# Kernel optimization log

Hardware: AMD Instinct MI355X
Metric: run time of the kernel (lower is better)

## Reference

```python
import jax, jax.numpy as jnp
import numpy as np

B, T, D = 2, 1024, 1024
H, HKV = 16, 8
HD = D // H           # 64
NREP = H // HKV       # 2
NLAYERS = 3
MAXKV = T * NLAYERS   # 3072
EPS = 1e-5


def setup_inputs() -> dict:
    key = jax.random.key(0)
    ks = jax.random.split(key, 8)
    # rotary tables over full accumulated-KV range
    inv_freq = 1.0 / (10000.0 ** (jnp.arange(0, HD, 2, dtype=jnp.float32) / HD))  # (HD/2,)
    t = jnp.arange(MAXKV, dtype=jnp.float32)
    freqs = jnp.outer(t, inv_freq)  # (MAXKV, HD/2)
    return {
        "x": jax.random.normal(ks[0], (B, T, D), jnp.float32),
        "cos": jnp.cos(freqs),
        "sin": jnp.sin(freqs),
        "q_w": jax.random.normal(ks[1], (NLAYERS, D, D), jnp.float32) * 0.02,
        "k_w": jax.random.normal(ks[2], (NLAYERS, D // NREP, D), jnp.float32) * 0.02,
        "v_w": jax.random.normal(ks[3], (NLAYERS, D // NREP, D), jnp.float32) * 0.02,
        "ln_w": jnp.ones((NLAYERS, D), jnp.float32),
        "lam": jax.random.normal(ks[4], (NLAYERS,), jnp.float32) * 0.1,
        "out_w": jax.random.normal(ks[5], (D, D), jnp.float32) * 0.02,
        "final_ln_w": jnp.ones((D,), jnp.float32),
        "alpha": jnp.ones((1,), jnp.float32),
    }


def rmsnorm(x, w):
    return x * jax.lax.rsqrt(jnp.mean(x * x, axis=-1, keepdims=True) + EPS) * w


def rope(x, cos, sin):
    # x: (B, L, h, HD); cos/sin: (MAXKV, HD/2); flash_attn non-interleaved rotary
    L = x.shape[1]
    c = jnp.concatenate([cos[:L], cos[:L]], axis=-1)[None, :, None, :]
    s = jnp.concatenate([sin[:L], sin[:L]], axis=-1)[None, :, None, :]
    x1, x2 = jnp.split(x, 2, axis=-1)
    rot = jnp.concatenate([-x2, x1], axis=-1)
    return x * c + rot * s


def reference(x, cos, sin, q_w, k_w, v_w, ln_w, lam, out_w, final_ln_w, alpha):
    scale = HD ** -0.5
    # lambda weights: layernorm over sigmoid of the 3 scalars (biased var, eps=1e-5)
    s = jax.nn.sigmoid(lam)
    lw = (s - s.mean()) * jax.lax.rsqrt(s.var() + EPS)
    qidx = jnp.arange(T)
    k_list, v_list = [], []
    acc = jnp.zeros_like(x)
    for i in range(NLAYERS):
        q = (x @ q_w[i].T).reshape(B, T, H, HD)
        k = (x @ k_w[i].T).reshape(B, T, HKV, HD)
        v = (x @ v_w[i].T).reshape(B, T, HKV, HD)
        k_list.append(k)
        v_list.append(v)
        K = jnp.concatenate(k_list, axis=1)  # (B, L, HKV, HD), L=(i+1)*T
        V = jnp.concatenate(v_list, axis=1)
        L = K.shape[1]
        qr = rope(q, cos, sin)
        Kr = rope(K, cos, sin)  # whole buffer re-rotated each layer, as in original
        Kr = jnp.repeat(Kr, NREP, axis=2)  # GQA expand
        Vr = jnp.repeat(V, NREP, axis=2)
        scores = jnp.einsum('bqhd,bkhd->bhqk', qr, Kr) * scale
        # flash_attn causal=True with kv_len > q_len aligns bottom-right
        mask = jnp.arange(L)[None, :] <= (qidx + (L - T))[:, None]
        scores = jnp.where(mask[None, None], scores, -jnp.inf)
        attn = jax.nn.softmax(scores, axis=-1)
        o = jnp.einsum('bhqk,bkhd->bqhd', attn, Vr).reshape(B, T, D)
        acc = acc + rmsnorm(o, ln_w[i]) * lw[i]
    out = rmsnorm(acc + alpha * x, final_ln_w)
    return out @ out_w.T
```

## Files before the change

kernel.cpp:

```cpp
#include <hip/hip_runtime.h>
#include <type_traits>
#include <utility>

typedef unsigned short u16;
typedef unsigned int u32;
typedef short short8 __attribute__((ext_vector_type(8)));
typedef short s16x4 __attribute__((ext_vector_type(4)));
typedef __bf16 bf16x8 __attribute__((ext_vector_type(8)));
typedef float floatx4 __attribute__((ext_vector_type(4)));

template <typename V, typename = void> struct MfmaTakes : std::false_type {};
template <typename V>
struct MfmaTakes<V, std::void_t<decltype(__builtin_amdgcn_mfma_f32_16x16x32_bf16(
    std::declval<V>(), std::declval<V>(), std::declval<floatx4>(), 0, 0, 0))>>
    : std::true_type {};

template <typename V>
__device__ __forceinline__ floatx4 mfma_impl(V a, V b, floatx4 c, std::true_type) {
  return __builtin_amdgcn_mfma_f32_16x16x32_bf16(a, b, c, 0, 0, 0);
}
template <typename V>
__device__ __forceinline__ floatx4 mfma_impl(V a, V b, floatx4 c, std::false_type) {
  return __builtin_amdgcn_mfma_f32_16x16x32_bf16(
      __builtin_bit_cast(bf16x8, a), __builtin_bit_cast(bf16x8, b), c, 0, 0, 0);
}
__device__ __forceinline__ floatx4 MFMA16(short8 a, short8 b, floatx4 c) {
  return mfma_impl<short8>(a, b, c, MfmaTakes<short8>{});
}

__device__ __forceinline__ floatx4 MFMAK16(s16x4 a, s16x4 b, floatx4 c) {
  return __builtin_amdgcn_mfma_f32_16x16x16bf16_1k(a, b, c, 0, 0, 0);
}

#if defined(__has_builtin)
#if __has_builtin(__builtin_amdgcn_exp2f)
#define EXP2(x) __builtin_amdgcn_exp2f(x)
#else
#define EXP2(x) exp2f(x)
#endif
#else
#define EXP2(x) exp2f(x)
#endif

__device__ __forceinline__ u16 f2bf(float f) {
  union { float f; unsigned u; } x; x.f = f;
  unsigned r = (x.u + 0x7fffu + ((x.u >> 16) & 1u)) >> 16;
  return (u16)r;
}
__device__ __forceinline__ float bf2f(u16 v) {
  union { unsigned u; float f; } x; x.u = ((unsigned)v) << 16; return x.f;
}
__device__ __forceinline__ u32 packbf(float lo, float hi) {
  return (__float_as_uint(hi) & 0xffff0000u) | (__float_as_uint(lo) >> 16);
}
__device__ __forceinline__ u32 pack2bf(float lo, float hi) {
  return ((u32)f2bf(hi) << 16) | (u32)f2bf(lo);
}

#if defined(__has_builtin)
#if __has_builtin(__builtin_amdgcn_global_load_lds)
#define HAS_GLLDS 1
#endif
#endif
__device__ __forceinline__ void stage16(const u16* g, u16* lbase, int lane) {
#ifdef HAS_GLLDS
  __builtin_amdgcn_global_load_lds(
      (__attribute__((address_space(1))) void*)(g),
      (__attribute__((address_space(3))) void*)(lbase), 16, 0, 0);
#else
  *(uint4*)(lbase + lane * 8) = *(const uint4*)g;
#endif
}

#define QSCALE 0.18033688011112042f

__global__ __launch_bounds__(256) void prep_kernel(
    const float* __restrict__ x, const float* __restrict__ qw,
    const float* __restrict__ kw, const float* __restrict__ vw,
    const float* __restrict__ outw, const float* __restrict__ lam,
    u16* __restrict__ xb, u16* __restrict__ wcat, u16* __restrict__ outwb,
    float* __restrict__ lwbuf) {
  size_t gid = (size_t)blockIdx.x * 256 + threadIdx.x;
  if (gid == 0) {
    float s0 = 1.f / (1.f + expf(-lam[0]));
    float s1 = 1.f / (1.f + expf(-lam[1]));
    float s2 = 1.f / (1.f + expf(-lam[2]));
    float mean = (s0 + s1 + s2) * (1.f / 3.f);
    float d0 = s0 - mean, d1 = s1 - mean, d2 = s2 - mean;
    float var = (d0 * d0 + d1 * d1 + d2 * d2) * (1.f / 3.f);
    float r = rsqrtf(var + 1e-5f);
    lwbuf[0] = d0 * r; lwbuf[1] = d1 * r; lwbuf[2] = d2 * r;
  }
  if (gid < 524288) {
    float4 v = ((const float4*)x)[gid];
    ushort4 o; o.x = f2bf(v.x); o.y = f2bf(v.y); o.z = f2bf(v.z); o.w = f2bf(v.w);
    ((ushort4*)xb)[gid] = o;
    return;
  }
  size_t g2 = gid - 524288;
  if (g2 < 1572864) {
    int col4 = (int)(g2 & 255);
    int n = (int)(g2 >> 8);
    int layer = n >> 11, r = n & 2047;
    const float* srcrow;
    if (r < 1024) srcrow = qw + ((size_t)(layer * 1024 + r) << 10);
    else if (r < 1536) srcrow = kw + ((size_t)(layer * 512 + (r - 1024)) << 10);
    else srcrow = vw + ((size_t)(layer * 512 + (r - 1536)) << 10);
    float4 v = ((const float4*)srcrow)[col4];
    ushort4 o; o.x = f2bf(v.x); o.y = f2bf(v.y); o.z = f2bf(v.z); o.w = f2bf(v.w);
    ((ushort4*)wcat)[g2] = o;
    return;
  }
  size_t g3 = g2 - 1572864;
  if (g3 < 262144) {
    float4 v = ((const float4*)outw)[g3];
    ushort4 o; o.x = f2bf(v.x); o.y = f2bf(v.y); o.z = f2bf(v.z); o.w = f2bf(v.w);
    ((ushort4*)outwb)[g3] = o;
  }
}

__global__ __launch_bounds__(256) void gemm_qkv(
    const u16* __restrict__ A, const u16* __restrict__ Bw,
    const float* __restrict__ cosb, const float* __restrict__ sinb,
    u16* __restrict__ qr, u16* __restrict__ kr, u16* __restrict__ vt) {
  __shared__ u16 As[128][64];
  __shared__ u16 Bs[128][64];
  const unsigned flat = blockIdx.x;
  const int bm = (flat >> 3) & 15;
  const int bn = ((flat >> 7) << 3) + (flat & 7);
  const int tid = threadIdx.x;
  const int wave = tid >> 6, lane = tid & 63;
  const int quad = lane >> 4, l16 = lane & 15;
  const int wm = wave & 1, wn = wave >> 1;
  const int srow = lane >> 3, skc = (lane & 7) * 8;
  floatx4 acc[4][4];
#pragma unroll
  for (int i = 0; i < 4; i++)
#pragma unroll
    for (int j = 0; j < 4; j++) { acc[i][j][0] = 0.f; acc[i][j][1] = 0.f; acc[i][j][2] = 0.f; acc[i][j][3] = 0.f; }
  const u16* Abase = A + (size_t)(bm * 128) * 1024;
  const u16* Bbase = Bw + (size_t)(bn * 128) * 1024;
  for (int k0 = 0; k0 < 1024; k0 += 64) {
    __syncthreads();
#pragma unroll
    for (int i = 0; i < 4; i++) {
      int ch = wave * 4 + i;
      stage16(Abase + (size_t)(ch * 8 + srow) * 1024 + k0 + skc, &As[ch * 8][0], lane);
      stage16(Bbase + (size_t)(ch * 8 + srow) * 1024 + k0 + skc, &Bs[ch * 8][0], lane);
    }
    __syncthreads();
#pragma unroll
    for (int kf = 0; kf < 2; kf++) {
      short8 af[4], bf[4];
#pragma unroll
      for (int mi = 0; mi < 4; mi++)
        af[mi] = *(const short8*)(&As[wm * 64 + mi * 16 + l16][kf * 32 + quad * 8]);
#pragma unroll
      for (int ni = 0; ni < 4; ni++)
        bf[ni] = *(const short8*)(&Bs[wn * 64 + ni * 16 + l16][kf * 32 + quad * 8]);
#pragma unroll
      for (int mi = 0; mi < 4; mi++)
#pragma unroll
        for (int ni = 0; ni < 4; ni++)
          acc[mi][ni] = MFMA16(af[mi], bf[ni], acc[mi][ni]);
    }
  }
  const int f0 = bn * 128 + wn * 64;
  const int lay = f0 >> 11;
  const int r0 = f0 & 2047;
  const int mrow0 = bm * 128 + wm * 64;
  if (r0 < 1024) {
    const int h = r0 >> 6;
#pragma unroll
    for (int mi = 0; mi < 4; mi++)
#pragma unroll
      for (int rr = 0; rr < 4; rr++) {
        int m = mrow0 + mi * 16 + quad * 4 + rr;
        int b = m >> 10, t = m & 1023;
        const float* cp = cosb + (size_t)t * 32;
        const float* sp = sinb + (size_t)t * 32;
        float c0 = cp[l16], s0 = sp[l16];
        float c1 = cp[16 + l16], s1 = sp[16 + l16];
        float x10 = acc[mi][0][rr], x20 = acc[mi][2][rr];
        float x11 = acc[mi][1][rr], x21 = acc[mi][3][rr];
        u16* row = qr + ((((size_t)lay * 2 + b) * 16 + h) * 1024 + t) * 64;
        row[l16]      = f2bf((x10 * c0 - x20 * s0) * QSCALE);
        row[16 + l16] = f2bf((x11 * c1 - x21 * s1) * QSCALE);
        row[32 + l16] = f2bf((x20 * c0 + x10 * s0) * QSCALE);
        row[48 + l16] = f2bf((x21 * c1 + x11 * s1) * QSCALE);
      }
  } else if (r0 < 1536) {
    const int hk = (r0 - 1024) >> 6;
#pragma unroll
    for (int mi = 0; mi < 4; mi++)
#pragma unroll
      for (int rr = 0; rr < 4; rr++) {
        int m = mrow0 + mi * 16 + quad * 4 + rr;
        int b = m >> 10, t = m & 1023;
        int pos = lay * 1024 + t;
        const float* cp = cosb + (size_t)pos * 32;
        const float* sp = sinb + (size_t)pos * 32;
        float c0 = cp[l16], s0 = sp[l16];
        float c1 = cp[16 + l16], s1 = sp[16 + l16];
        float x10 = acc[mi][0][rr], x20 = acc[mi][2][rr];
        float x11 = acc[mi][1][rr], x21 = acc[mi][3][rr];
        u16* row = kr + (((size_t)(b * 8 + hk)) * 3072 + pos) * 64;
        row[l16]      = f2bf(x10 * c0 - x20 * s0);
        row[16 + l16] = f2bf(x11 * c1 - x21 * s1);
        row[32 + l16] = f2bf(x20 * c0 + x10 * s0);
        row[48 + l16] = f2bf(x21 * c1 + x11 * s1);
      }
  } else {
    const int hv = (r0 - 1536) >> 6;
#pragma unroll
    for (int mi = 0; mi < 4; mi++) {
      int m0 = mrow0 + mi * 16 + quad * 4;
      int b = m0 >> 10;
      int pos0 = lay * 1024 + (m0 & 1023);
      u16* colbase = vt + ((size_t)(b * 8 + hv) * 64) * 3072 + pos0;
#pragma unroll
      for (int ni = 0; ni < 4; ni++) {
        int d = ni * 16 + l16;
        uint2 st;
        st.x = pack2bf(acc[mi][ni][0], acc[mi][ni][1]);
        st.y = pack2bf(acc[mi][ni][2], acc[mi][ni][3]);
        *(uint2*)(colbase + (size_t)d * 3072) = st;
      }
    }
  }
}

__global__ __launch_bounds__(256) void gemm_bt(
    const u16* __restrict__ A, const u16* __restrict__ Bw,
    float* __restrict__ C, int N, int K) {
  __shared__ u16 As[64][72];
  __shared__ u16 Bs[64][72];
  const int bm = blockIdx.x, bn = blockIdx.y;
  const int tid = threadIdx.x;
  const int wave = tid >> 6, lane = tid & 63;
  const int quad = lane >> 4, l16 = lane & 15;
  const int lr = tid >> 2, lc = (tid & 3) << 4;
  floatx4 acc[4];
#pragma unroll
  for (int i = 0; i < 4; i++) { acc[i][0] = 0.f; acc[i][1] = 0.f; acc[i][2] = 0.f; acc[i][3] = 0.f; }
  const u16* Arow = A + (size_t)(bm * 64 + lr) * K;
  const u16* Brow = Bw + (size_t)(bn * 64 + lr) * K;
  for (int k0 = 0; k0 < K; k0 += 64) {
    __syncthreads();
    *(uint4*)(&As[lr][lc])     = *(const uint4*)(Arow + k0 + lc);
    *(uint4*)(&As[lr][lc + 8]) = *(const uint4*)(Arow + k0 + lc + 8);
    *(uint4*)(&Bs[lr][lc])     = *(const uint4*)(Brow + k0 + lc);
    *(uint4*)(&Bs[lr][lc + 8]) = *(const uint4*)(Brow + k0 + lc + 8);
    __syncthreads();
    const int mrow = wave * 16 + l16;
    short8 a0 = *(const short8*)(&As[mrow][quad * 8]);
    short8 a1 = *(const short8*)(&As[mrow][32 + quad * 8]);
#pragma unroll
    for (int ns = 0; ns < 4; ns++) {
      short8 b0 = *(const short8*)(&Bs[ns * 16 + l16][quad * 8]);
      short8 b1 = *(const short8*)(&Bs[ns * 16 + l16][32 + quad * 8]);
      acc[ns] = MFMA16(a0, b0, acc[ns]);
      acc[ns] = MFMA16(a1, b1, acc[ns]);
    }
  }
#pragma unroll
  for (int ns = 0; ns < 4; ns++)
#pragma unroll
    for (int r = 0; r < 4; r++) {
      int row = bm * 64 + wave * 16 + quad * 4 + r;
      int col = bn * 64 + ns * 16 + l16;
      C[(size_t)row * N + col] = acc[ns][r];
    }
}

__global__ __launch_bounds__(512) void attn_v12(
    const u16* __restrict__ qr, const u16* __restrict__ kr,
    const u16* __restrict__ vt, u16* __restrict__ obS,
    float* __restrict__ lbufp) {
  __shared__ __align__(16) u16 smem[18432];
  u16* KtB = smem;
  u16* VtB = smem + 9216;
  const unsigned flat = blockIdx.x;
  const int xcd = (int)(flat & 7);
  const int m = (int)(flat >> 3);
  const int qtile = m / 12;
  const int g = m - qtile * 12;
  const int pid = g * 8 + xcd;
  const int z = pid >> 4;
  const int rb = pid & 15;
  const int b = rb >> 3, j = rb & 7;
  const int lay = (z == 5) ? 0 : ((z == 0 || z == 4) ? 1 : 2);
  const int n64 = lay * 16 + qtile * 2 + 2;
  int kt0, kt1;
  if (lay == 0) { kt0 = 0; kt1 = n64; }
  else if (lay == 1) { int hf = n64 >> 1; kt0 = (z == 0) ? 0 : hf; kt1 = (z == 0) ? hf : n64; }
  else {
    int t1 = n64 / 3, t2 = (2 * n64) / 3;
    kt0 = (z == 1) ? 0 : ((z == 2) ? t1 : t2);
    kt1 = (z == 1) ? t1 : ((z == 2) ? t2 : n64);
  }
  const int maskkt = lay * 16 + qtile * 2;
  const int tid = threadIdx.x, wave = tid >> 6, lane = tid & 63;
  const int quad = lane >> 4, l16 = lane & 15;
  const int hw = wave >> 2, wq = wave & 3;
  const int h = j * 2 + hw;
  const int qeffbase = lay * 1024 + qtile * 128 + wq * 32;
  const u16* qpb = qr + ((((size_t)lay * 2 + b) * 16 + h) * 1024
                         + qtile * 128 + wq * 32 + l16) * 64 + quad * 8;
  short8 qf[2][2];
  qf[0][0] = *(const short8*)(qpb);
  qf[0][1] = *(const short8*)(qpb + 32);
  qf[1][0] = *(const short8*)(qpb + 1024);
  qf[1][1] = *(const short8*)(qpb + 1056);
  const s16x4 ones4 = {16256, 16256, 16256, 16256};
  floatx4 oacc[2][4];
#pragma unroll
  for (int nt = 0; nt < 2; nt++)
#pragma unroll
    for (int dt = 0; dt < 4; dt++) { oacc[nt][dt][0] = 0.f; oacc[nt][dt][1] = 0.f; oacc[nt][dt][2] = 0.f; oacc[nt][dt][3] = 0.f; }
  floatx4 lacc[2];
  lacc[0][0] = 0.f; lacc[0][1] = 0.f; lacc[0][2] = 0.f; lacc[0][3] = 0.f;
  lacc[1] = lacc[0];
  const bool isK = (tid < 256);
  const int t2i = tid & 255;
  const int sr = t2i >> 2, sc = (t2i & 3) * 8;
  const u16* gp = isK
      ? kr + ((size_t)(b * 8 + j) * 3072 + (size_t)kt0 * 64 + sr) * 64 + sc
      : vt + ((size_t)(b * 8 + j) * 64 + sr) * 3072 + (size_t)kt0 * 64 + sc;
  const size_t gstep = isK ? 4096 : 64;
  u16* lbase = isK ? &KtB[sr * 72 + sc] : &VtB[sr * 72 + sc];
  uint4 gA = *(const uint4*)gp;
  uint4 gB = *(const uint4*)(gp + 32);
  *(uint4*)(lbase)      = gA;
  *(uint4*)(lbase + 32) = gB;
  gp += gstep;
  if (kt0 + 1 < kt1) { gA = *(const uint4*)gp; gB = *(const uint4*)(gp + 32); }
  for (int kt = kt0; kt < kt1; kt++) {
    const int p = (kt - kt0) & 1;
    __syncthreads();
    if (kt + 1 < kt1) {
      u16* lb1 = lbase + (p ? 0 : 4608);
      *(uint4*)(lb1)      = gA;
      *(uint4*)(lb1 + 32) = gB;
      gp += gstep;
      if (kt + 2 < kt1) { gA = *(const uint4*)gp; gB = *(const uint4*)(gp + 32); }
    }
    const bool needmask = (kt >= maskkt);
    const u16* Ktp = &KtB[p * 4608];
    const u16* Vtp = &VtB[p * 4608];
#pragma unroll
    for (int mp = 0; mp < 2; mp++) {
      uint2 pk[2][2];
#pragma unroll
      for (int mh = 0; mh < 2; mh++) {
        const int mt = mp * 2 + mh;
        short8 kfa = *(const short8*)(&Ktp[(mt * 16 + l16) * 72 + quad * 8]);
        short8 kfb = *(const short8*)(&Ktp[(mt * 16 + l16) * 72 + 32 + quad * 8]);
        const int keyb = kt * 64 + mt * 16 + quad * 4;
#pragma unroll
        for (int nt = 0; nt < 2; nt++) {
          floatx4 s; s[0] = 0.f; s[1] = 0.f; s[2] = 0.f; s[3] = 0.f;
          s = MFMA16(kfa, qf[nt][0], s);
          s = MFMA16(kfb, qf[nt][1], s);
          float p0 = EXP2(s[0]), p1 = EXP2(s[1]);
          float p2 = EXP2(s[2]), p3 = EXP2(s[3]);
          if (needmask) {
            int qpos = qeffbase + nt * 16 + l16;
            if (keyb + 0 > qpos) p0 = 0.f;
            if (keyb + 1 > qpos) p1 = 0.f;
            if (keyb + 2 > qpos) p2 = 0.f;
            if (keyb + 3 > qpos) p3 = 0.f;
          }
          pk[mh][nt].x = packbf(p0, p1);
          pk[mh][nt].y = packbf(p2, p3);
        }
      }
      s16x4 p0f0 = __builtin_bit_cast(s16x4, pk[0][0]);
      s16x4 p1f0 = __builtin_bit_cast(s16x4, pk[1][0]);
      s16x4 p0f1 = __builtin_bit_cast(s16x4, pk[0][1]);
      s16x4 p1f1 = __builtin_bit_cast(s16x4, pk[1][1]);
      __builtin_amdgcn_s_setprio(1);
      lacc[0] = MFMAK16(ones4, p0f0, lacc[0]);
      lacc[0] = MFMAK16(ones4, p1f0, lacc[0]);
      lacc[1] = MFMAK16(ones4, p0f1, lacc[1]);
      lacc[1] = MFMAK16(ones4, p1f1, lacc[1]);
#pragma unroll
      for (int dt = 0; dt < 4; dt++) {
        s16x4 v0 = *(const s16x4*)(&Vtp[(dt * 16 + l16) * 72 + mp * 32 + quad * 4]);
        s16x4 v1 = *(const s16x4*)(&Vtp[(dt * 16 + l16) * 72 + mp * 32 + 16 + quad * 4]);
        oacc[0][dt] = MFMAK16(v0, p0f0, oacc[0][dt]);
        oacc[0][dt] = MFMAK16(v1, p1f0, oacc[0][dt]);
        oacc[1][dt] = MFMAK16(v0, p0f1, oacc[1][dt]);
        oacc[1][dt] = MFMAK16(v1, p1f1, oacc[1][dt]);
      }
      __builtin_amdgcn_s_setprio(0);
    }
  }
  __syncthreads();
  float* Pf = (float*)smem + wave * 320;
  const int tt = lane >> 2, dd = (lane & 3) << 2;
#pragma unroll
  for (int nt = 0; nt < 2; nt++) {
    int t = qtile * 128 + wq * 32 + nt * 16 + l16;
    if (quad == 0)
      lbufp[((size_t)z * 2048 + b * 1024 + t) * 16 + h] = lacc[nt][0];
    int t2 = qtile * 128 + wq * 32 + nt * 16 + tt;
    u16* orow = obS + ((size_t)(z * 2 + b) * 1024 + t2) * 1024 + h * 64 + dd;
#pragma unroll
    for (int dt = 0; dt < 4; dt++) {
      *(floatx4*)(&Pf[l16 * 20 + quad * 4]) = oacc[nt][dt];
      floatx4 val = *(const floatx4*)(&Pf[tt * 20 + dd]);
      uint2 st; st.x = pack2bf(val[0], val[1]); st.y = pack2bf(val[2], val[3]);
      *(uint2*)(orow + dt * 16) = st;
    }
  }
}

__device__ __forceinline__ float block_sum(float v, float* red) {
  v += __shfl_xor(v, 32); v += __shfl_xor(v, 16); v += __shfl_xor(v, 8);
  v += __shfl_xor(v, 4);  v += __shfl_xor(v, 2);  v += __shfl_xor(v, 1);
  __syncthreads();
  if ((threadIdx.x & 63) == 0) red[threadIdx.x >> 6] = v;
  __syncthreads();
  return red[0] + red[1] + red[2] + red[3];
}

__global__ __launch_bounds__(256) void fused_norm(
    const u16* __restrict__ obS, const float* __restrict__ lbufp,
    const float* __restrict__ x, const float* __restrict__ lnw,
    const float* __restrict__ lwbuf, const float* __restrict__ flnw,
    const float* __restrict__ alphap, u16* __restrict__ y) {
  __shared__ float red[4];
  const int row = blockIdx.x, tid = threadIdx.x;
  float a[4] = {0.f, 0.f, 0.f, 0.f};
  const int nsl[3] = {1, 2, 3};
  const int sl[3][3] = {{5, 0, 0}, {0, 4, 0}, {1, 2, 3}};
#pragma unroll
  for (int l = 0; l < 3; l++) {
    float o0 = 0.f, o1 = 0.f, o2 = 0.f, o3 = 0.f, ls = 0.f;
#pragma unroll
    for (int si = 0; si < 3; si++) {
      if (si >= nsl[l]) break;
      int z = sl[l][si];
      uint2 v = ((const uint2*)(obS + ((size_t)z * 2048 + row) * 1024))[tid];
      o0 += bf2f((u16)(v.x & 0xffff)); o1 += bf2f((u16)(v.x >> 16));
      o2 += bf2f((u16)(v.y & 0xffff)); o3 += bf2f((u16)(v.y >> 16));
      ls += lbufp[((size_t)z * 2048 + row) * 16 + (tid >> 4)];
    }
    float linv = 1.f / ls;
    float v0 = o0 * linv, v1 = o1 * linv, v2 = o2 * linv, v3 = o3 * linv;
    float ss = v0 * v0 + v1 * v1 + v2 * v2 + v3 * v3;
    ss = block_sum(ss, red);
    float rstd = rsqrtf(ss * (1.f / 1024.f) + 1e-5f);
    float lw = lwbuf[l];
    float4 w = ((const float4*)(lnw + (size_t)l * 1024))[tid];
    a[0] += v0 * rstd * w.x * lw;
    a[1] += v1 * rstd * w.y * lw;
    a[2] += v2 * rstd * w.z * lw;
    a[3] += v3 * rstd * w.w * lw;
  }
  const float aa = alphap[0];
  float4 xv = ((const float4*)(x + (size_t)row * 1024))[tid];
  float v0 = a[0] + aa * xv.x, v1 = a[1] + aa * xv.y;
  float v2 = a[2] + aa * xv.z, v3 = a[3] + aa * xv.w;
  float ss = v0 * v0 + v1 * v1 + v2 * v2 + v3 * v3;
  ss = block_sum(ss, red);
  float rstd = rsqrtf(ss * (1.f / 1024.f) + 1e-5f);
  float4 fw = ((const float4*)flnw)[tid];
  ushort4 o;
  o.x = f2bf(v0 * rstd * fw.x); o.y = f2bf(v1 * rstd * fw.y);
  o.z = f2bf(v2 * rstd * fw.z); o.w = f2bf(v3 * rstd * fw.w);
  ((ushort4*)(y + (size_t)row * 1024))[tid] = o;
}

extern "C" void kernel_launch(void* const* d_in, const int* in_sizes, int n_in,
                              void* d_out, int out_size, void* d_ws, size_t ws_size,
                              hipStream_t stream) {
  const float* x     = (const float*)d_in[0];
  const float* cosb  = (const float*)d_in[1];
  const float* sinb  = (const float*)d_in[2];
  const float* qw    = (const float*)d_in[3];
  const float* kw    = (const float*)d_in[4];
  const float* vw    = (const float*)d_in[5];
  const float* lnw   = (const float*)d_in[6];
  const float* lam   = (const float*)d_in[7];
  const float* outw  = (const float*)d_in[8];
  const float* flnw  = (const float*)d_in[9];
  const float* alphap= (const float*)d_in[10];
  float* out = (float*)d_out;
  char* ws = (char*)d_ws;
  u16*   xb    = (u16*)  (ws + 0);
  u16*   wcat  = (u16*)  (ws + 4194304);
  u16*   obS   = (u16*)  (ws + 0);
  u16*   outwb = (u16*)  (ws + 25165824);
  float* lwbuf = (float*)(ws + 27262976);
  u16*   qr    = (u16*)  (ws + 27264000);
  u16*   kr    = (u16*)  (ws + 39846912);
  u16*   vt    = (u16*)  (ws + 46138368);
  float* lbufp = (float*)(ws + 52429824);
  u16*   yb    = (u16*)  (ws + 53216256);

  prep_kernel<<<9216, 256, 0, stream>>>(x, qw, kw, vw, outw, lam, xb, wcat, outwb, lwbuf);
  gemm_qkv<<<768, 256, 0, stream>>>(xb, wcat, cosb, sinb, qr, kr, vt);
  attn_v12<<<768, 512, 0, stream>>>(qr, kr, vt, obS, lbufp);
  fused_norm<<<2048, 256, 0, stream>>>(obS, lbufp, x, lnw, lwbuf, flnw, alphap, yb);
  gemm_bt<<<dim3(32, 16), 256, 0, stream>>>(yb, outwb, out, 1024, 1024);
}
```

Before: 248.4 us.

## Use 4 waves with 64 query rows each and skip fully masked key tiles

The attention block drops from 8 waves to 4, and each wave now handles 64 query rows instead of 32. Every K fragment read from LDS is therefore reused across twice as many MFMAs, and staging loads are spread over fewer threads. Each wave now skips key tiles that lie entirely beyond its causal boundary, not just masking them. The cost is more accumulator registers per wave, fewer resident waves, and uneven work between waves within a block.

```diff
diff --git a/kernel.cpp b/kernel.cpp
--- a/kernel.cpp
+++ b/kernel.cpp
@@ -273,7 +273,7 @@
     }
 }
 
-__global__ __launch_bounds__(512) void attn_v12(
+__global__ __launch_bounds__(256) void attn_v13(
     const u16* __restrict__ qr, const u16* __restrict__ kr,
     const u16* __restrict__ vt, u16* __restrict__ obS,
     float* __restrict__ lbufp) {
@@ -299,58 +299,75 @@
     kt0 = (z == 1) ? 0 : ((z == 2) ? t1 : t2);
     kt1 = (z == 1) ? t1 : ((z == 2) ? t2 : n64);
   }
-  const int maskkt = lay * 16 + qtile * 2;
   const int tid = threadIdx.x, wave = tid >> 6, lane = tid & 63;
   const int quad = lane >> 4, l16 = lane & 15;
-  const int hw = wave >> 2, wq = wave & 3;
+  const int hw = wave >> 1, wq = wave & 1;
   const int h = j * 2 + hw;
-  const int qeffbase = lay * 1024 + qtile * 128 + wq * 32;
+  const int qeffbase = lay * 1024 + qtile * 128 + wq * 64;
+  const int maskw = lay * 16 + qtile * 2 + wq;
   const u16* qpb = qr + ((((size_t)lay * 2 + b) * 16 + h) * 1024
-                         + qtile * 128 + wq * 32 + l16) * 64 + quad * 8;
-  short8 qf[2][2];
-  qf[0][0] = *(const short8*)(qpb);
-  qf[0][1] = *(const short8*)(qpb + 32);
-  qf[1][0] = *(const short8*)(qpb + 1024);
-  qf[1][1] = *(const short8*)(qpb + 1056);
+                         + qtile * 128 + wq * 64 + l16) * 64 + quad * 8;
+  short8 qf[4][2];
+#pragma unroll
+  for (int nt = 0; nt < 4; nt++) {
+    qf[nt][0] = *(const short8*)(qpb + nt * 1024);
+    qf[nt][1] = *(const short8*)(qpb + nt * 1024 + 32);
+  }
   const s16x4 ones4 = {16256, 16256, 16256, 16256};
-  floatx4 oacc[2][4];
-#pragma unroll
-  for (int nt = 0; nt < 2; nt++)
-#pragma unroll
-    for (int dt = 0; dt < 4; dt++) { oacc[nt][dt][0] = 0.f; oacc[nt][dt][1] = 0.f; oacc[nt][dt][2] = 0.f; oacc[nt][dt][3] = 0.f; }
-  floatx4 lacc[2];
-  lacc[0][0] = 0.f; lacc[0][1] = 0.f; lacc[0][2] = 0.f; lacc[0][3] = 0.f;
-  lacc[1] = lacc[0];
-  const bool isK = (tid < 256);
-  const int t2i = tid & 255;
-  const int sr = t2i >> 2, sc = (t2i & 3) * 8;
+  floatx4 oacc[4][4];
+  floatx4 lacc[4];
+#pragma unroll
+  for (int nt = 0; nt < 4; nt++) {
+    lacc[nt][0] = 0.f; lacc[nt][1] = 0.f; lacc[nt][2] = 0.f; lacc[nt][3] = 0.f;
+#pragma unroll
+    for (int dt = 0; dt < 4; dt++) {
+      oacc[nt][dt][0] = 0.f; oacc[nt][dt][1] = 0.f;
+      oacc[nt][dt][2] = 0.f; oacc[nt][dt][3] = 0.f;
+    }
+  }
+  const bool isK = (tid < 128);
+  const int t2i = tid & 127;
+  const int sr = t2i >> 1, scb = (t2i & 1) * 32;
   const u16* gp = isK
-      ? kr + ((size_t)(b * 8 + j) * 3072 + (size_t)kt0 * 64 + sr) * 64 + sc
-      : vt + ((size_t)(b * 8 + j) * 64 + sr) * 3072 + (size_t)kt0 * 64 + sc;
+      ? kr + ((size_t)(b * 8 + j) * 3072 + (size_t)kt0 * 64 + sr) * 64 + scb
+      : vt + ((size_t)(b * 8 + j) * 64 + sr) * 3072 + (size_t)kt0 * 64 + scb;
   const size_t gstep = isK ? 4096 : 64;
-  u16* lbase = isK ? &KtB[sr * 72 + sc] : &VtB[sr * 72 + sc];
-  uint4 gA = *(const uint4*)gp;
-  uint4 gB = *(const uint4*)(gp + 32);
-  *(uint4*)(lbase)      = gA;
-  *(uint4*)(lbase + 32) = gB;
+  u16* lbase = (isK ? KtB : VtB) + sr * 72 + scb;
+  uint4 g0 = *(const uint4*)(gp);
+  uint4 g1 = *(const uint4*)(gp + 8);
+  uint4 g2 = *(const uint4*)(gp + 16);
+  uint4 g3 = *(const uint4*)(gp + 24);
+  *(uint4*)(lbase)      = g0;
+  *(uint4*)(lbase + 8)  = g1;
+  *(uint4*)(lbase + 16) = g2;
+  *(uint4*)(lbase + 24) = g3;
   gp += gstep;
-  if (kt0 + 1 < kt1) { gA = *(const uint4*)gp; gB = *(const uint4*)(gp + 32); }
+  if (kt0 + 1 < kt1) {
+    g0 = *(const uint4*)(gp);      g1 = *(const uint4*)(gp + 8);
+    g2 = *(const uint4*)(gp + 16); g3 = *(const uint4*)(gp + 24);
+  }
   for (int kt = kt0; kt < kt1; kt++) {
     const int p = (kt - kt0) & 1;
     __syncthreads();
     if (kt + 1 < kt1) {
       u16* lb1 = lbase + (p ? 0 : 4608);
-      *(uint4*)(lb1)      = gA;
-      *(uint4*)(lb1 + 32) = gB;
+      *(uint4*)(lb1)      = g0;
+      *(uint4*)(lb1 + 8)  = g1;
+      *(uint4*)(lb1 + 16) = g2;
+      *(uint4*)(lb1 + 24) = g3;
       gp += gstep;
-      if (kt + 2 < kt1) { gA = *(const uint4*)gp; gB = *(const uint4*)(gp + 32); }
-    }
-    const bool needmask = (kt >= maskkt);
+      if (kt + 2 < kt1) {
+        g0 = *(const uint4*)(gp);      g1 = *(const uint4*)(gp + 8);
+        g2 = *(const uint4*)(gp + 16); g3 = *(const uint4*)(gp + 24);
+      }
+    }
+    if (kt > maskw) continue;
+    const bool needmask = (kt == maskw);
     const u16* Ktp = &KtB[p * 4608];
     const u16* Vtp = &VtB[p * 4608];
 #pragma unroll
     for (int mp = 0; mp < 2; mp++) {
-      uint2 pk[2][2];
+      uint2 pk[2][4];
 #pragma unroll
       for (int mh = 0; mh < 2; mh++) {
         const int mt = mp * 2 + mh;
@@ -358,7 +375,7 @@
         short8 kfb = *(const short8*)(&Ktp[(mt * 16 + l16) * 72 + 32 + quad * 8]);
         const int keyb = kt * 64 + mt * 16 + quad * 4;
 #pragma unroll
-        for (int nt = 0; nt < 2; nt++) {
+        for (int nt = 0; nt < 4; nt++) {
           floatx4 s; s[0] = 0.f; s[1] = 0.f; s[2] = 0.f; s[3] = 0.f;
           s = MFMA16(kfa, qf[nt][0], s);
           s = MFMA16(kfb, qf[nt][1], s);
@@ -375,23 +392,27 @@
           pk[mh][nt].y = packbf(p2, p3);
         }
       }
-      s16x4 p0f0 = __builtin_bit_cast(s16x4, pk[0][0]);
-      s16x4 p1f0 = __builtin_bit_cast(s16x4, pk[1][0]);
-      s16x4 p0f1 = __builtin_bit_cast(s16x4, pk[0][1]);
-      s16x4 p1f1 = __builtin_bit_cast(s16x4, pk[1][1]);
+      s16x4 p0f[4], p1f[4];
+#pragma unroll
+      for (int nt = 0; nt < 4; nt++) {
+        p0f[nt] = __builtin_bit_cast(s16x4, pk[0][nt]);
+        p1f[nt] = __builtin_bit_cast(s16x4, pk[1][nt]);
+      }
       __builtin_amdgcn_s_setprio(1);
-      lacc[0] = MFMAK16(ones4, p0f0, lacc[0]);
-      lacc[0] = MFMAK16(ones4, p1f0, lacc[0]);
-      lacc[1] = MFMAK16(ones4, p0f1, lacc[1]);
-      lacc[1] = MFMAK16(ones4, p1f1, lacc[1]);
+#pragma unroll
+      for (int nt = 0; nt < 4; nt++) {
+        lacc[nt] = MFMAK16(ones4, p0f[nt], lacc[nt]);
+        lacc[nt] = MFMAK16(ones4, p1f[nt], lacc[nt]);
+      }
 #pragma unroll
       for (int dt = 0; dt < 4; dt++) {
         s16x4 v0 = *(const s16x4*)(&Vtp[(dt * 16 + l16) * 72 + mp * 32 + quad * 4]);
         s16x4 v1 = *(const s16x4*)(&Vtp[(dt * 16 + l16) * 72 + mp * 32 + 16 + quad * 4]);
-        oacc[0][dt] = MFMAK16(v0, p0f0, oacc[0][dt]);
-        oacc[0][dt] = MFMAK16(v1, p1f0, oacc[0][dt]);
-        oacc[1][dt] = MFMAK16(v0, p0f1, oacc[1][dt]);
-        oacc[1][dt] = MFMAK16(v1, p1f1, oacc[1][dt]);
+#pragma unroll
+        for (int nt = 0; nt < 4; nt++) {
+          oacc[nt][dt] = MFMAK16(v0, p0f[nt], oacc[nt][dt]);
+          oacc[nt][dt] = MFMAK16(v1, p1f[nt], oacc[nt][dt]);
+        }
       }
       __builtin_amdgcn_s_setprio(0);
     }
@@ -400,11 +421,11 @@
   float* Pf = (float*)smem + wave * 320;
   const int tt = lane >> 2, dd = (lane & 3) << 2;
 #pragma unroll
-  for (int nt = 0; nt < 2; nt++) {
-    int t = qtile * 128 + wq * 32 + nt * 16 + l16;
+  for (int nt = 0; nt < 4; nt++) {
+    int t = qtile * 128 + wq * 64 + nt * 16 + l16;
     if (quad == 0)
       lbufp[((size_t)z * 2048 + b * 1024 + t) * 16 + h] = lacc[nt][0];
-    int t2 = qtile * 128 + wq * 32 + nt * 16 + tt;
+    int t2 = qtile * 128 + wq * 64 + nt * 16 + tt;
     u16* orow = obS + ((size_t)(z * 2 + b) * 1024 + t2) * 1024 + h * 64 + dd;
 #pragma unroll
     for (int dt = 0; dt < 4; dt++) {
@@ -502,7 +523,7 @@
 
   prep_kernel<<<9216, 256, 0, stream>>>(x, qw, kw, vw, outw, lam, xb, wcat, outwb, lwbuf);
   gemm_qkv<<<768, 256, 0, stream>>>(xb, wcat, cosb, sinb, qr, kr, vt);
-  attn_v12<<<768, 512, 0, stream>>>(qr, kr, vt, obS, lbufp);
+  attn_v13<<<768, 256, 0, stream>>>(qr, kr, vt, obS, lbufp);
   fused_norm<<<2048, 256, 0, stream>>>(obS, lbufp, x, lnw, lwbuf, flnw, alphap, yb);
   gemm_bt<<<dim3(32, 16), 256, 0, stream>>>(yb, outwb, out, 1024, 1024);
 }
```

Result: slower. 301.1 us (+21.2%).
